# Optimization experiments

Measured on AMD Instinct MI355X. Metric: run time of the kernel, lower is better.

Reference implementation:

```python
import jax, jax.numpy as jnp
import numpy as np

N = 100000      # number of nodes (z rows) and z0 rows
E = 1000000     # number of edges
EMB = 128       # args.emb_size


def setup_inputs() -> dict:
    key = jax.random.key(0)
    k1, k2, k3, k4, k5 = jax.random.split(key, 5)
    z = jax.random.normal(k1, (N, EMB), dtype=jnp.float32)
    z0 = jax.random.normal(k2, (N, EMB), dtype=jnp.float32)
    edge_index = jax.random.randint(k3, (2, E), 0, N, dtype=jnp.int64)
    # torch Linear weights: [out_features, in_features]
    Wq = jax.random.normal(k4, (EMB, 2 * EMB), dtype=jnp.float32) * (1.0 / np.sqrt(2 * EMB))
    Wo = jax.random.normal(k5, (1, 2 * EMB), dtype=jnp.float32) * (1.0 / np.sqrt(2 * EMB))
    bo = jnp.zeros((1,), dtype=jnp.float32)
    return {"z": z, "edge_index": edge_index, "z0": z0, "Wq": Wq, "Wo": Wo, "bo": bo}


def reference(z, edge_index, z0, Wq, Wo, bo):
    # qid: per-edge max of the two endpoint ids, shifted to start at 0
    qid = jnp.max(edge_index[0:2], axis=0)
    qid = qid - qid.min()
    emb1 = z[edge_index[0]]            # [E, EMB]
    emb2 = z[edge_index[1]]            # [E, EMB]
    x0 = jnp.concatenate([emb2, z0[qid]], axis=-1) @ Wq.T   # [E, EMB]
    out = jnp.concatenate([emb1, x0], axis=-1) @ Wo.T + bo  # [E, 1]
    return out.reshape(-1)
```

## Files before the change

### kernel.cpp

```cpp
#include <hip/hip_runtime.h>
#include <climits>

#define EMB 128
#define EMB2 256

typedef float v4f __attribute__((ext_vector_type(4)));
typedef int   v4i __attribute__((ext_vector_type(4)));

__global__ void prep_kernel(const float* __restrict__ Wq,
                            const float* __restrict__ Wo,
                            const int* __restrict__ ei, int E,
                            float* __restrict__ weff,
                            unsigned int* __restrict__ qmin) {
    if (blockIdx.x == 0) {
        int k = threadIdx.x;
        float acc = 0.f;
#pragma unroll 8
        for (int j = 0; j < EMB; ++j)
            acc += Wo[EMB + j] * Wq[j * EMB2 + k];
        weff[k] = acc;
        return;
    }
    unsigned int m = 0xFFFFFFFFu;
    int nvec = E >> 2;
    int nthreads = (gridDim.x - 1) * blockDim.x;
    int tid = (blockIdx.x - 1) * blockDim.x + threadIdx.x;
    const v4i* r0 = (const v4i*)ei;
    const v4i* r1 = (const v4i*)(ei + E);
    for (int v = tid; v < nvec; v += nthreads) {
        v4i a = r0[v];
        v4i b = r1[v];
        unsigned m0 = (unsigned)max(a.x, b.x), m1 = (unsigned)max(a.y, b.y);
        unsigned m2 = (unsigned)max(a.z, b.z), m3 = (unsigned)max(a.w, b.w);
        m = min(m, min(min(m0, m1), min(m2, m3)));
    }
    if (blockIdx.x == 1 && threadIdx.x < (E & 3)) {
        int e = (nvec << 2) + threadIdx.x;
        m = min(m, (unsigned)max(ei[e], ei[e + E]));
    }
    for (int off = 32; off; off >>= 1) {
        unsigned o = (unsigned)__shfl_xor((int)m, off, 64);
        m = min(m, o);
    }
    __shared__ unsigned sm[4];
    int wid = threadIdx.x >> 6;
    if ((threadIdx.x & 63) == 0) sm[wid] = m;
    __syncthreads();
    if (threadIdx.x == 0) {
        unsigned r = min(min(sm[0], sm[1]), min(sm[2], sm[3]));
        atomicMin(qmin, r);
    }
}

__global__ void node_dots_kernel(const float* __restrict__ z,
                                 const float* __restrict__ z0,
                                 const float* __restrict__ Wo,
                                 const float* __restrict__ weff,
                                 v4f* __restrict__ tab,
                                 int N) {
    int gtid = blockIdx.x * blockDim.x + threadIdx.x;
    int wave = gtid >> 6;
    int lane = gtid & 63;
    int sub = lane >> 5;
    int c = lane & 31;
    int row = wave * 2 + sub;
    if (row >= N) return;

    v4f w1 = ((const v4f*)Wo)[c];
    v4f wa = ((const v4f*)weff)[c];
    v4f wb = ((const v4f*)weff)[32 + c];

    v4f zv  = __builtin_nontemporal_load(((const v4f*)(z  + (size_t)row * EMB)) + c);
    v4f z0v = __builtin_nontemporal_load(((const v4f*)(z0 + (size_t)row * EMB)) + c);

    float p1 = w1.x * zv.x + w1.y * zv.y + w1.z * zv.z + w1.w * zv.w;
    float p2 = wa.x * zv.x + wa.y * zv.y + wa.z * zv.z + wa.w * zv.w;
    float p3 = wb.x * z0v.x + wb.y * z0v.y + wb.z * z0v.z + wb.w * z0v.w;

#pragma unroll
    for (int off = 16; off; off >>= 1) {
        p1 += __shfl_xor(p1, off, 64);
        p2 += __shfl_xor(p2, off, 64);
        p3 += __shfl_xor(p3, off, 64);
    }
    if (c == 0) {
        v4f r; r.x = p1; r.y = p2; r.z = p3; r.w = 0.f;
        tab[row] = r;
    }
}

__global__ void edge_out_kernel(const int* __restrict__ ei,
                                const v4f* __restrict__ tab,
                                const int* __restrict__ qminp,
                                const float* __restrict__ bo,
                                float* __restrict__ out, int E) {
    int qmin = *qminp;
    float b0 = *bo;
    int t = blockIdx.x * blockDim.x + threadIdx.x;
    int e4 = t << 2;
    if (e4 + 3 < E) {
        v4i a = *(const v4i*)(ei + e4);
        v4i b = *(const v4i*)(ei + E + e4);
        v4f r;
        r.x = tab[a.x].x + tab[b.x].y + tab[max(a.x, b.x) - qmin].z + b0;
        r.y = tab[a.y].x + tab[b.y].y + tab[max(a.y, b.y) - qmin].z + b0;
        r.z = tab[a.z].x + tab[b.z].y + tab[max(a.z, b.z) - qmin].z + b0;
        r.w = tab[a.w].x + tab[b.w].y + tab[max(a.w, b.w) - qmin].z + b0;
        __builtin_nontemporal_store(r, (v4f*)(out + e4));
    } else {
        for (int e = e4; e < E; ++e) {
            int a = ei[e], b = ei[e + E];
            out[e] = tab[a].x + tab[b].y + tab[max(a, b) - qmin].z + b0;
        }
    }
}

extern "C" void kernel_launch(void* const* d_in, const int* in_sizes, int n_in,
                              void* d_out, int out_size, void* d_ws, size_t ws_size,
                              hipStream_t stream) {
    const float* z    = (const float*)d_in[0];
    const int*   ei   = (const int*)d_in[1];
    const float* z0   = (const float*)d_in[2];
    const float* Wq   = (const float*)d_in[3];
    const float* Wo   = (const float*)d_in[4];
    const float* bo   = (const float*)d_in[5];
    float* out = (float*)d_out;

    int N = in_sizes[0] / EMB;
    int E = in_sizes[1] / 2;

    v4f* tab = (v4f*)d_ws;
    float* weff = (float*)(tab + N);
    unsigned int* qmin = (unsigned int*)(weff + EMB2);

    hipMemsetAsync(qmin, 0xFF, sizeof(unsigned int), stream);

    prep_kernel<<<513, 256, 0, stream>>>(Wq, Wo, ei, E, weff, qmin);

    int pairs = (N + 1) / 2;
    int blocksC = (pairs + 3) / 4;
    node_dots_kernel<<<blocksC, 256, 0, stream>>>(z, z0, Wo, weff, tab, N);

    int threadsD = (E + 3) / 4;
    int blocksD = (threadsD + 255) / 256;
    edge_out_kernel<<<blocksD, 256, 0, stream>>>(ei, tab, (const int*)qmin, bo, out, E);
}
```

Before: 158.7 us.

## Fuse qid-min, node dots and edge gather into one cooperative persistent kernel

Replaces the memset, the prep kernel, the node-dot kernel and the edge-output kernel with a small weff kernel plus one cooperative kernel of fixed grid size. That kernel computes per-block qid minima into slots, then computes the node table with a grid-stride loop, does a grid.sync, reduces the slots in every block and runs the edge gather. The aim is to cut launch gaps and the atomic between stages. In exchange it adds grid-wide sync overhead, relies on all 1024 blocks being co-resident, and limits parallelism to a fixed persistent grid.

```diff
diff --git a/kernel.cpp b/kernel.cpp
--- a/kernel.cpp
+++ b/kernel.cpp
@@ -1,117 +1,129 @@
 #include <hip/hip_runtime.h>
+#include <hip/hip_cooperative_groups.h>
 #include <climits>
 
 #define EMB 128
 #define EMB2 256
+#define GRID_BLOCKS 1024
+#define BLOCK_THREADS 256
 
 typedef float v4f __attribute__((ext_vector_type(4)));
 typedef int   v4i __attribute__((ext_vector_type(4)));
 
-__global__ void prep_kernel(const float* __restrict__ Wq,
+__global__ void weff_kernel(const float* __restrict__ Wq,
                             const float* __restrict__ Wo,
-                            const int* __restrict__ ei, int E,
-                            float* __restrict__ weff,
-                            unsigned int* __restrict__ qmin) {
-    if (blockIdx.x == 0) {
-        int k = threadIdx.x;
-        float acc = 0.f;
+                            float* __restrict__ weff) {
+    int k = threadIdx.x;
+    float acc = 0.f;
 #pragma unroll 8
-        for (int j = 0; j < EMB; ++j)
-            acc += Wo[EMB + j] * Wq[j * EMB2 + k];
-        weff[k] = acc;
-        return;
-    }
-    unsigned int m = 0xFFFFFFFFu;
-    int nvec = E >> 2;
-    int nthreads = (gridDim.x - 1) * blockDim.x;
-    int tid = (blockIdx.x - 1) * blockDim.x + threadIdx.x;
+    for (int j = 0; j < EMB; ++j)
+        acc += Wo[EMB + j] * Wq[j * EMB2 + k];
+    weff[k] = acc;
+}
+
+__global__ void fused_kernel(const float* __restrict__ z,
+                             const float* __restrict__ z0,
+                             const int* __restrict__ ei, int E,
+                             const float* __restrict__ Wo,
+                             const float* __restrict__ weff,
+                             const float* __restrict__ bo,
+                             v4f* __restrict__ tab, int N,
+                             int* __restrict__ slots,
+                             float* __restrict__ out) {
+    cooperative_groups::grid_group grid = cooperative_groups::this_grid();
+    const int gtid = blockIdx.x * BLOCK_THREADS + threadIdx.x;
+    const int ntot = GRID_BLOCKS * BLOCK_THREADS;
+    const int nvec = E >> 2;
     const v4i* r0 = (const v4i*)ei;
     const v4i* r1 = (const v4i*)(ei + E);
-    for (int v = tid; v < nvec; v += nthreads) {
+
+    int m = INT_MAX;
+    for (int v = gtid; v < nvec; v += ntot) {
         v4i a = r0[v];
         v4i b = r1[v];
-        unsigned m0 = (unsigned)max(a.x, b.x), m1 = (unsigned)max(a.y, b.y);
-        unsigned m2 = (unsigned)max(a.z, b.z), m3 = (unsigned)max(a.w, b.w);
+        int m0 = max(a.x, b.x), m1 = max(a.y, b.y);
+        int m2 = max(a.z, b.z), m3 = max(a.w, b.w);
         m = min(m, min(min(m0, m1), min(m2, m3)));
     }
-    if (blockIdx.x == 1 && threadIdx.x < (E & 3)) {
-        int e = (nvec << 2) + threadIdx.x;
-        m = min(m, (unsigned)max(ei[e], ei[e + E]));
+    if (gtid < (E & 3)) {
+        int e = (nvec << 2) + gtid;
+        m = min(m, max(ei[e], ei[e + E]));
     }
-    for (int off = 32; off; off >>= 1) {
-        unsigned o = (unsigned)__shfl_xor((int)m, off, 64);
-        m = min(m, o);
+#pragma unroll
+    for (int off = 32; off; off >>= 1)
+        m = min(m, __shfl_xor(m, off, 64));
+    __shared__ int sm[4];
+    if ((threadIdx.x & 63) == 0) sm[threadIdx.x >> 6] = m;
+    __syncthreads();
+    if (threadIdx.x == 0)
+        slots[blockIdx.x] = min(min(sm[0], sm[1]), min(sm[2], sm[3]));
+
+    {
+        int wave = gtid >> 6, lane = gtid & 63;
+        int nwaves = ntot >> 6;
+        int sub = lane >> 5;
+        int c = lane & 31;
+        v4f w1 = ((const v4f*)Wo)[c];
+        v4f wa = ((const v4f*)weff)[c];
+        v4f wb = ((const v4f*)weff)[32 + c];
+        int npairs = (N + 1) >> 1;
+        for (int p = wave; p < npairs; p += nwaves) {
+            int row = 2 * p + sub;
+            v4f zv, z0v;
+            if (row < N) {
+                zv  = __builtin_nontemporal_load(((const v4f*)(z  + (size_t)row * EMB)) + c);
+                z0v = __builtin_nontemporal_load(((const v4f*)(z0 + (size_t)row * EMB)) + c);
+            } else {
+                zv = (v4f)0.f; z0v = (v4f)0.f;
+            }
+            float p1 = w1.x * zv.x + w1.y * zv.y + w1.z * zv.z + w1.w * zv.w;
+            float p2 = wa.x * zv.x + wa.y * zv.y + wa.z * zv.z + wa.w * zv.w;
+            float p3 = wb.x * z0v.x + wb.y * z0v.y + wb.z * z0v.z + wb.w * z0v.w;
+#pragma unroll
+            for (int off = 16; off; off >>= 1) {
+                p1 += __shfl_xor(p1, off, 64);
+                p2 += __shfl_xor(p2, off, 64);
+                p3 += __shfl_xor(p3, off, 64);
+            }
+            if (c == 0 && row < N) {
+                v4f r; r.x = p1; r.y = p2; r.z = p3; r.w = 0.f;
+                tab[row] = r;
+            }
+        }
     }
-    __shared__ unsigned sm[4];
-    int wid = threadIdx.x >> 6;
-    if ((threadIdx.x & 63) == 0) sm[wid] = m;
-    __syncthreads();
-    if (threadIdx.x == 0) {
-        unsigned r = min(min(sm[0], sm[1]), min(sm[2], sm[3]));
-        atomicMin(qmin, r);
+
+    grid.sync();
+
+    __shared__ int sq[5];
+    {
+        int t = threadIdx.x;
+        int mm = min(min(slots[t], slots[t + 256]),
+                     min(slots[t + 512], slots[t + 768]));
+#pragma unroll
+        for (int off = 32; off; off >>= 1)
+            mm = min(mm, __shfl_xor(mm, off, 64));
+        if ((t & 63) == 0) sq[t >> 6] = mm;
+        __syncthreads();
+        if (t == 0) sq[4] = min(min(sq[0], sq[1]), min(sq[2], sq[3]));
+        __syncthreads();
     }
-}
+    const int qmin = sq[4];
+    const float b0 = *bo;
 
-__global__ void node_dots_kernel(const float* __restrict__ z,
-                                 const float* __restrict__ z0,
-                                 const float* __restrict__ Wo,
-                                 const float* __restrict__ weff,
-                                 v4f* __restrict__ tab,
-                                 int N) {
-    int gtid = blockIdx.x * blockDim.x + threadIdx.x;
-    int wave = gtid >> 6;
-    int lane = gtid & 63;
-    int sub = lane >> 5;
-    int c = lane & 31;
-    int row = wave * 2 + sub;
-    if (row >= N) return;
-
-    v4f w1 = ((const v4f*)Wo)[c];
-    v4f wa = ((const v4f*)weff)[c];
-    v4f wb = ((const v4f*)weff)[32 + c];
-
-    v4f zv  = __builtin_nontemporal_load(((const v4f*)(z  + (size_t)row * EMB)) + c);
-    v4f z0v = __builtin_nontemporal_load(((const v4f*)(z0 + (size_t)row * EMB)) + c);
-
-    float p1 = w1.x * zv.x + w1.y * zv.y + w1.z * zv.z + w1.w * zv.w;
-    float p2 = wa.x * zv.x + wa.y * zv.y + wa.z * zv.z + wa.w * zv.w;
-    float p3 = wb.x * z0v.x + wb.y * z0v.y + wb.z * z0v.z + wb.w * z0v.w;
-
-#pragma unroll
-    for (int off = 16; off; off >>= 1) {
-        p1 += __shfl_xor(p1, off, 64);
-        p2 += __shfl_xor(p2, off, 64);
-        p3 += __shfl_xor(p3, off, 64);
-    }
-    if (c == 0) {
-        v4f r; r.x = p1; r.y = p2; r.z = p3; r.w = 0.f;
-        tab[row] = r;
-    }
-}
-
-__global__ void edge_out_kernel(const int* __restrict__ ei,
-                                const v4f* __restrict__ tab,
-                                const int* __restrict__ qminp,
-                                const float* __restrict__ bo,
-                                float* __restrict__ out, int E) {
-    int qmin = *qminp;
-    float b0 = *bo;
-    int t = blockIdx.x * blockDim.x + threadIdx.x;
-    int e4 = t << 2;
-    if (e4 + 3 < E) {
-        v4i a = *(const v4i*)(ei + e4);
-        v4i b = *(const v4i*)(ei + E + e4);
+    for (int v = gtid; v < nvec; v += ntot) {
+        v4i a = r0[v];
+        v4i b = r1[v];
         v4f r;
         r.x = tab[a.x].x + tab[b.x].y + tab[max(a.x, b.x) - qmin].z + b0;
         r.y = tab[a.y].x + tab[b.y].y + tab[max(a.y, b.y) - qmin].z + b0;
         r.z = tab[a.z].x + tab[b.z].y + tab[max(a.z, b.z) - qmin].z + b0;
         r.w = tab[a.w].x + tab[b.w].y + tab[max(a.w, b.w) - qmin].z + b0;
-        __builtin_nontemporal_store(r, (v4f*)(out + e4));
-    } else {
-        for (int e = e4; e < E; ++e) {
-            int a = ei[e], b = ei[e + E];
-            out[e] = tab[a].x + tab[b].y + tab[max(a, b) - qmin].z + b0;
-        }
+        __builtin_nontemporal_store(r, (v4f*)(out + ((size_t)v << 2)));
+    }
+    if (gtid < (E & 3)) {
+        int e = (nvec << 2) + gtid;
+        int a = ei[e], b = ei[e + E];
+        out[e] = tab[a].x + tab[b].y + tab[max(a, b) - qmin].z + b0;
     }
 }
 
@@ -129,19 +141,18 @@
     int N = in_sizes[0] / EMB;
     int E = in_sizes[1] / 2;
 
-    v4f* tab = (v4f*)d_ws;
+    v4f*  tab   = (v4f*)d_ws;
     float* weff = (float*)(tab + N);
-    unsigned int* qmin = (unsigned int*)(weff + EMB2);
+    int*  slots = (int*)(weff + EMB2);
 
-    hipMemsetAsync(qmin, 0xFF, sizeof(unsigned int), stream);
+    weff_kernel<<<1, EMB2, 0, stream>>>(Wq, Wo, weff);
 
-    prep_kernel<<<513, 256, 0, stream>>>(Wq, Wo, ei, E, weff, qmin);
-
-    int pairs = (N + 1) / 2;
-    int blocksC = (pairs + 3) / 4;
-    node_dots_kernel<<<blocksC, 256, 0, stream>>>(z, z0, Wo, weff, tab, N);
-
-    int threadsD = (E + 3) / 4;
-    int blocksD = (threadsD + 255) / 256;
-    edge_out_kernel<<<blocksD, 256, 0, stream>>>(ei, tab, (const int*)qmin, bo, out, E);
+    void* kargs[] = {
+        (void*)&z, (void*)&z0, (void*)&ei, (void*)&E,
+        (void*)&Wo, (void*)&weff, (void*)&bo,
+        (void*)&tab, (void*)&N, (void*)&slots, (void*)&out
+    };
+    hipLaunchCooperativeKernel((const void*)fused_kernel,
+                               dim3(GRID_BLOCKS), dim3(BLOCK_THREADS),
+                               kargs, 0, stream);
 }
```

Result: slower. 250.6 us (+57.9%).
